# Optimization experiments

Hardware: AMD Instinct MI355X
Metric: run time of the kernel (lower is better)

Reference implementation:

```python
import jax, jax.numpy as jnp
import numpy as np

N = 50000
E = 625000
D_IN, D_HID, D_OUT = 128, 128, 64


def setup_inputs() -> dict:
    key = jax.random.key(0)
    k1, k2, k3, k4 = jax.random.split(key, 4)
    x = jax.random.normal(k1, (N, D_IN), dtype=jnp.float32)
    edge_index = jax.random.randint(k2, (2, E), 0, N, dtype=jnp.int32)
    # Glorot-ish init for linear weights (PyG lin has no bias; bias added after agg)
    W1 = jax.random.normal(k3, (D_HID, D_IN), dtype=jnp.float32) / np.sqrt(D_IN)
    b1 = jnp.zeros((D_HID,), dtype=jnp.float32)
    W2 = jax.random.normal(k4, (D_OUT, D_HID), dtype=jnp.float32) / np.sqrt(D_HID)
    b2 = jnp.zeros((D_OUT,), dtype=jnp.float32)
    return {"x": x, "edge_index": edge_index, "W1": W1, "b1": b1, "W2": W2, "b2": b2}


def _gcn_conv(x, W, b, src, dst, n):
    # GCNConv: h = x @ W^T; out[dst] += norm * h[src]; out += b
    # src/dst already include self-loops; symmetric normalization deg^{-1/2}.
    ones = jnp.ones(src.shape[0], dtype=x.dtype)
    deg = jax.ops.segment_sum(ones, dst, num_segments=n)
    dinv = jnp.where(deg > 0, jax.lax.rsqrt(deg), 0.0)
    norm = dinv[src] * dinv[dst]                      # [E+N]
    h = x @ W.T                                        # [N, d_out]
    msg = norm[:, None] * h[src]                       # [E+N, d_out]
    out = jax.ops.segment_sum(msg, dst, num_segments=n)
    return out + b


def reference(x, edge_index, W1, b1, W2, b2):
    n = x.shape[0]
    loops = jnp.arange(n, dtype=edge_index.dtype)
    src = jnp.concatenate([edge_index[0], loops])      # add self-loops
    dst = jnp.concatenate([edge_index[1], loops])
    h = _gcn_conv(x, W1, b1, src, dst, n)
    h = jax.nn.relu(h)
    out = _gcn_conv(h, W2, b2, src, dst, n)
    return out
```

## Files before the change

kernel.cpp:

```cpp
#include <hip/hip_runtime.h>
#include <hip/hip_bf16.h>


typedef __attribute__((ext_vector_type(8))) __bf16 bf16x8;
typedef __attribute__((ext_vector_type(8))) unsigned short ushort8;
typedef __attribute__((ext_vector_type(4))) float floatx4;

static __device__ __forceinline__ float bf2f(unsigned short s) {
    unsigned u = ((unsigned)s) << 16;
    return __builtin_bit_cast(float, u);
}
static __device__ __forceinline__ unsigned short f2bf(float f) {
    unsigned u = __builtin_bit_cast(unsigned, f);
    unsigned r = (u + 0x7FFFu + ((u >> 16) & 1u)) >> 16;
    return (unsigned short)r;
}
static __device__ __forceinline__ void ld8f(const void* p, size_t idx, int isbf, float* o) {
    if (isbf) {
        ushort8 t = __builtin_bit_cast(ushort8, *(const int4*)((const unsigned short*)p + idx));
        #pragma unroll
        for (int j = 0; j < 8; ++j) o[j] = bf2f(t[j]);
    } else {
        const float* f = (const float*)p + idx;
        float4 a = *(const float4*)f;
        float4 b = *(const float4*)(f + 4);
        o[0]=a.x; o[1]=a.y; o[2]=a.z; o[3]=a.w; o[4]=b.x; o[5]=b.y; o[6]=b.z; o[7]=b.w;
    }
}
static __device__ __forceinline__ int4 ld8frag(const void* p, size_t idx, int isbf) {
    if (isbf) {
        return *(const int4*)((const unsigned short*)p + idx);
    } else {
        const float* f = (const float*)p + idx;
        float4 a = *(const float4*)f;
        float4 b = *(const float4*)(f + 4);
        ushort8 t;
        t[0]=f2bf(a.x); t[1]=f2bf(a.y); t[2]=f2bf(a.z); t[3]=f2bf(a.w);
        t[4]=f2bf(b.x); t[5]=f2bf(b.y); t[6]=f2bf(b.z); t[7]=f2bf(b.w);
        return __builtin_bit_cast(int4, t);
    }
}
static __device__ __forceinline__ float bread(const void* p, int i, int isbf) {
    return isbf ? bf2f(((const unsigned short*)p)[i]) : ((const float*)p)[i];
}

__global__ void k_detect(const unsigned* __restrict__ xw, int* flag) {
    __shared__ int red[256];
    int t = threadIdx.x;
    int cnt = 0;
    #pragma unroll
    for (int i = 0; i < 16; ++i) {
        unsigned w = xw[t * 16 + i];
        unsigned exp = (w >> 7) & 0xFFu;
        cnt += (exp <= 0x84u) ? 1 : 0;
    }
    red[t] = cnt;
    __syncthreads();
    for (int s = 128; s > 0; s >>= 1) {
        if (t < s) red[t] += red[t + s];
        __syncthreads();
    }
    if (t == 0) flag[0] = (red[0] >= 3686) ? 1 : 0;
}

__global__ void k_zero(int* cnt, int n) {
    int i = blockIdx.x * 256 + threadIdx.x;
    if (i < n) cnt[i] = 0;
}
__global__ void k_count(const int* __restrict__ dst, int* __restrict__ cnt, int E) {
    int e = blockIdx.x * 256 + threadIdx.x;
    if (e < E) atomicAdd(&cnt[dst[e]], 1);
}
__global__ __launch_bounds__(1024) void k_scan(
    const int* __restrict__ cnt, int* __restrict__ off, int* __restrict__ cursor,
    float* __restrict__ dinv, int N)
{
    __shared__ int wtot[16];
    __shared__ int woff[16];
    __shared__ int s_carry;
    int t = threadIdx.x, lane = t & 63, wid = t >> 6;
    if (t == 0) s_carry = 0;
    __syncthreads();
    int nchunk = (N + 1023) / 1024;
    for (int c = 0; c < nchunk; ++c) {
        int i = c * 1024 + t;
        int v = (i < N) ? cnt[i] : 0;
        int x = v;
        #pragma unroll
        for (int s = 1; s < 64; s <<= 1) {
            int u = __shfl_up(x, s, 64);
            if (lane >= s) x += u;
        }
        if (lane == 63) wtot[wid] = x;
        __syncthreads();
        if (wid == 0) {
            int tv = (lane < 16) ? wtot[lane] : 0;
            int y = tv;
            #pragma unroll
            for (int s = 1; s < 16; s <<= 1) {
                int u = __shfl_up(y, s, 64);
                if (lane >= s) y += u;
            }
            if (lane < 16) woff[lane] = y - tv;
        }
        __syncthreads();
        int carry = s_carry;
        if (i < N) {
            int excl = carry + woff[wid] + (x - v);
            off[i] = excl;
            cursor[i] = excl;
            dinv[i] = rsqrtf(1.0f + (float)v);
        }
        __syncthreads();
        if (t == 0) s_carry = carry + woff[15] + wtot[15];
        __syncthreads();
    }
    if (t == 0) off[N] = s_carry;
}
__global__ void k_scatter(const int* __restrict__ src, const int* __restrict__ dst,
                          int* __restrict__ cursor, int* __restrict__ bucket, int E) {
    int e = blockIdx.x * 256 + threadIdx.x;
    if (e >= E) return;
    int pos = atomicAdd(&cursor[dst[e]], 1);
    bucket[pos] = src[e];
}

__global__ __launch_bounds__(256) void k_gather1(
    const void* __restrict__ x, const float* __restrict__ dinv,
    const int* __restrict__ off, const int* __restrict__ bucket,
    float* __restrict__ buf, int N, const int* __restrict__ flag)
{
    int isbf = *flag;
    int gid = blockIdx.x * 256 + threadIdx.x;
    int node = gid >> 4, p = gid & 15;
    if (node >= N) return;
    float di = dinv[node];
    float acc[8], v[8];
    ld8f(x, (size_t)node * 128 + p * 8, isbf, v);
    float w0 = di * di;
    #pragma unroll
    for (int j = 0; j < 8; ++j) acc[j] = w0 * v[j];
    int s0 = off[node], s1 = off[node + 1];
    for (int it = s0; it < s1; ++it) {
        int s = bucket[it];
        float w = di * dinv[s];
        ld8f(x, (size_t)s * 128 + p * 8, isbf, v);
        #pragma unroll
        for (int j = 0; j < 8; ++j) acc[j] += w * v[j];
    }
    float* o = &buf[(size_t)node * 128 + p * 8];
    float4 a = {acc[0], acc[1], acc[2], acc[3]};
    float4 b = {acc[4], acc[5], acc[6], acc[7]};
    *(float4*)o = a;
    *(float4*)(o + 4) = b;
}

__global__ __launch_bounds__(256) void k_gemm1(
    float* buf, const void* __restrict__ W1, const void* __restrict__ b1,
    int N, const int* __restrict__ flag)
{
    int isbf = *flag;
    __shared__ int4 lds[2048];
    int tid = threadIdx.x;
    for (int u = tid; u < 2048; u += 256) {
        int nt = u >> 8, kt = (u >> 6) & 3, lane = u & 63;
        int so = (nt * 16 + (lane & 15)) * 128 + kt * 32 + ((lane >> 4) << 3);
        lds[u] = ld8frag(W1, so, isbf);
    }
    __syncthreads();

    int wave = tid >> 6, lane = tid & 63;
    int ntile = (N + 15) >> 4;
    int tile = blockIdx.x * 4 + wave;
    if (tile >= ntile) return;
    int m = lane & 15, quad = lane >> 4;

    int arow = tile * 16 + m;
    if (arow >= N) arow = N - 1;
    bf16x8 a[4];
    for (int kt = 0; kt < 4; ++kt) {
        const float* p = &buf[(size_t)arow * 128 + kt * 32 + quad * 8];
        float4 f0 = *(const float4*)p;
        float4 f1 = *(const float4*)(p + 4);
        ushort8 t;
        t[0]=f2bf(f0.x); t[1]=f2bf(f0.y); t[2]=f2bf(f0.z); t[3]=f2bf(f0.w);
        t[4]=f2bf(f1.x); t[5]=f2bf(f1.y); t[6]=f2bf(f1.z); t[7]=f2bf(f1.w);
        a[kt] = __builtin_bit_cast(bf16x8, t);
    }

    floatx4 acc[8];
    floatx4 z = {0.f, 0.f, 0.f, 0.f};
    for (int nt = 0; nt < 8; ++nt) acc[nt] = z;
    for (int kt = 0; kt < 4; ++kt)
        for (int nt = 0; nt < 8; ++nt) {
            bf16x8 b = __builtin_bit_cast(bf16x8, lds[nt * 256 + kt * 64 + lane]);
            acc[nt] = __builtin_amdgcn_mfma_f32_16x16x32_bf16(a[kt], b, acc[nt], 0, 0, 0);
        }

    unsigned short* h1 = (unsigned short*)buf;
    int rbase = tile * 16 + quad * 4;
    for (int nt = 0; nt < 8; ++nt) {
        int col = nt * 16 + m;
        float bb = bread(b1, col, isbf);
        for (int r = 0; r < 4; ++r) {
            int orow = rbase + r;
            if (orow < N) {
                float v = acc[nt][r] + bb;
                h1[(size_t)orow * 256 + col] = f2bf(fmaxf(v, 0.f));
            }
        }
    }
}

__global__ __launch_bounds__(256) void k_gemm2(
    float* buf, const void* __restrict__ W2, int N, const int* __restrict__ flag)
{
    int isbf = *flag;
    __shared__ int4 lds[1024];
    int tid = threadIdx.x;
    for (int u = tid; u < 1024; u += 256) {
        int nt = u >> 8, kt = (u >> 6) & 3, lane = u & 63;
        int so = (nt * 16 + (lane & 15)) * 128 + kt * 32 + ((lane >> 4) << 3);
        lds[u] = ld8frag(W2, so, isbf);
    }
    __syncthreads();

    int wave = tid >> 6, lane = tid & 63;
    int ntile = (N + 15) >> 4;
    int tile = blockIdx.x * 4 + wave;
    if (tile >= ntile) return;
    int m = lane & 15, quad = lane >> 4;

    const unsigned short* h1 = (const unsigned short*)buf;
    int arow = tile * 16 + m;
    if (arow >= N) arow = N - 1;
    bf16x8 a[4];
    for (int kt = 0; kt < 4; ++kt)
        a[kt] = __builtin_bit_cast(bf16x8, *(const int4*)&h1[(size_t)arow * 256 + kt * 32 + quad * 8]);

    floatx4 acc[4];
    floatx4 z = {0.f, 0.f, 0.f, 0.f};
    for (int nt = 0; nt < 4; ++nt) acc[nt] = z;
    for (int kt = 0; kt < 4; ++kt)
        for (int nt = 0; nt < 4; ++nt) {
            bf16x8 b = __builtin_bit_cast(bf16x8, lds[nt * 256 + kt * 64 + lane]);
            acc[nt] = __builtin_amdgcn_mfma_f32_16x16x32_bf16(a[kt], b, acc[nt], 0, 0, 0);
        }

    unsigned short* h2 = (unsigned short*)buf;
    int rbase = tile * 16 + quad * 4;
    for (int nt = 0; nt < 4; ++nt) {
        int col = nt * 16 + m;
        for (int r = 0; r < 4; ++r) {
            int orow = rbase + r;
            if (orow < N)
                h2[(size_t)orow * 256 + col] = f2bf(acc[nt][r]);
        }
    }
}

__global__ __launch_bounds__(256) void k_gather2(
    const float* __restrict__ buf, const float* __restrict__ dinv,
    const int* __restrict__ off, const int* __restrict__ bucket,
    const void* __restrict__ b2, void* __restrict__ out, int N,
    const int* __restrict__ flag)
{
    int isbf = *flag;
    int gid = blockIdx.x * 256 + threadIdx.x;
    int node = gid >> 3, p = gid & 7;
    if (node >= N) return;
    const unsigned short* h2 = (const unsigned short*)buf;
    float di = dinv[node];
    float acc[8];
    {
        ushort8 t = __builtin_bit_cast(ushort8, *(const int4*)&h2[(size_t)node * 256 + p * 8]);
        float w0 = di * di;
        #pragma unroll
        for (int j = 0; j < 8; ++j) acc[j] = w0 * bf2f(t[j]);
    }
    int s0 = off[node], s1 = off[node + 1];
    for (int it = s0; it < s1; ++it) {
        int s = bucket[it];
        float w = di * dinv[s];
        ushort8 t = __builtin_bit_cast(ushort8, *(const int4*)&h2[(size_t)s * 256 + p * 8]);
        #pragma unroll
        for (int j = 0; j < 8; ++j) acc[j] += w * bf2f(t[j]);
    }
    #pragma unroll
    for (int j = 0; j < 8; ++j) acc[j] += bread(b2, p * 8 + j, isbf);
    if (isbf) {
        ushort8 o;
        #pragma unroll
        for (int j = 0; j < 8; ++j) o[j] = f2bf(acc[j]);
        *(int4*)((unsigned short*)out + (size_t)node * 64 + p * 8) = __builtin_bit_cast(int4, o);
    } else {
        float* fo = (float*)out + (size_t)node * 64 + p * 8;
        float4 a = {acc[0], acc[1], acc[2], acc[3]};
        float4 b = {acc[4], acc[5], acc[6], acc[7]};
        *(float4*)fo = a;
        *(float4*)(fo + 4) = b;
    }
}

extern "C" void kernel_launch(void* const* d_in, const int* in_sizes, int n_in,
                              void* d_out, int out_size, void* d_ws, size_t ws_size,
                              hipStream_t stream) {
    const void* x  = d_in[0];
    const int*  ei = (const int*)d_in[1];
    const void* W1 = d_in[2];
    const void* b1 = d_in[3];
    const void* W2 = d_in[4];
    const void* b2 = d_in[5];

    int N = in_sizes[0] / 128;
    int E = in_sizes[1] / 2;
    const int* srcI = ei;
    const int* dstI = ei + E;

    char* base = (char*)d_ws;
    size_t o = 0;
    auto take = [&](size_t bytes) { size_t r = o; o += (bytes + 255) & ~(size_t)255; return r; };
    int*   flag   = (int*)  (base + take(4));
    int*   cnt    = (int*)  (base + take((size_t)N * 4));
    int*   off    = (int*)  (base + take((size_t)(N + 1) * 4));
    int*   cursor = (int*)  (base + take((size_t)N * 4));
    float* dinv   = (float*)(base + take((size_t)N * 4));
    int*   bucket = (int*)  (base + take((size_t)E * 4));
    float* buf    = (float*)(base + take((size_t)N * 512));

    int ntile = (N + 15) / 16;
    int gemmBlocks = (ntile + 3) / 4;

    k_detect<<<1, 256, 0, stream>>>((const unsigned*)x, flag);
    k_zero<<<(N + 255) / 256, 256, 0, stream>>>(cnt, N);
    k_count<<<(E + 255) / 256, 256, 0, stream>>>(dstI, cnt, E);
    k_scan<<<1, 1024, 0, stream>>>(cnt, off, cursor, dinv, N);
    k_scatter<<<(E + 255) / 256, 256, 0, stream>>>(srcI, dstI, cursor, bucket, E);
    k_gather1<<<(N * 16 + 255) / 256, 256, 0, stream>>>(x, dinv, off, bucket, buf, N, flag);
    k_gemm1<<<gemmBlocks, 256, 0, stream>>>(buf, W1, b1, N, flag);
    k_gemm2<<<gemmBlocks, 256, 0, stream>>>(buf, W2, N, flag);
    k_gather2<<<(N * 8 + 255) / 256, 256, 0, stream>>>(buf, dinv, off, bucket, b2, d_out, N, flag);
}
```

Baseline: 298.1 us.

## Parallelize degree prefix scan across blocks and unroll gather loops by two

Replaces the single-block serial-chunk prefix scan over node degrees with a three-kernel reduce/scan/downsweep scheme spread across many blocks. Each thread now handles four elements. The neighbor gather loops in both aggregation kernels are unrolled by two so two independent row loads are in flight per iteration. This trades one long single-workgroup kernel for three short launches plus extra workspace, and raises register use in the gathers.

```diff
diff --git a/kernel.cpp b/kernel.cpp
--- a/kernel.cpp
+++ b/kernel.cpp
@@ -71,52 +71,88 @@
     int e = blockIdx.x * 256 + threadIdx.x;
     if (e < E) atomicAdd(&cnt[dst[e]], 1);
 }
-__global__ __launch_bounds__(1024) void k_scan(
-    const int* __restrict__ cnt, int* __restrict__ off, int* __restrict__ cursor,
-    float* __restrict__ dinv, int N)
-{
-    __shared__ int wtot[16];
-    __shared__ int woff[16];
-    __shared__ int s_carry;
-    int t = threadIdx.x, lane = t & 63, wid = t >> 6;
-    if (t == 0) s_carry = 0;
-    __syncthreads();
-    int nchunk = (N + 1023) / 1024;
-    for (int c = 0; c < nchunk; ++c) {
-        int i = c * 1024 + t;
-        int v = (i < N) ? cnt[i] : 0;
+
+__global__ __launch_bounds__(256) void k_scanA(
+    const int* __restrict__ cnt, int* __restrict__ partial, int N)
+{
+    int b = blockIdx.x, t = threadIdx.x;
+    int base = b * 1024 + t * 4;
+    int s = 0;
+    if (base + 3 < N) {
+        int4 v = *(const int4*)&cnt[base];
+        s = v.x + v.y + v.z + v.w;
+    } else {
+        for (int j = 0; j < 4; ++j) { int i = base + j; if (i < N) s += cnt[i]; }
+    }
+    #pragma unroll
+    for (int d = 1; d < 64; d <<= 1) s += __shfl_down(s, d, 64);
+    __shared__ int ws[4];
+    int lane = t & 63, wid = t >> 6;
+    if (lane == 0) ws[wid] = s;
+    __syncthreads();
+    if (t == 0) partial[b] = ws[0] + ws[1] + ws[2] + ws[3];
+}
+__global__ void k_scanB(const int* __restrict__ partial, int* __restrict__ prefix, int nb) {
+    int lane = threadIdx.x;
+    int carry = 0;
+    int nch = (nb + 63) / 64;
+    for (int c = 0; c < nch; ++c) {
+        int i = c * 64 + lane;
+        int v = (i < nb) ? partial[i] : 0;
         int x = v;
         #pragma unroll
-        for (int s = 1; s < 64; s <<= 1) {
-            int u = __shfl_up(x, s, 64);
-            if (lane >= s) x += u;
-        }
-        if (lane == 63) wtot[wid] = x;
-        __syncthreads();
-        if (wid == 0) {
-            int tv = (lane < 16) ? wtot[lane] : 0;
-            int y = tv;
-            #pragma unroll
-            for (int s = 1; s < 16; s <<= 1) {
-                int u = __shfl_up(y, s, 64);
-                if (lane >= s) y += u;
-            }
-            if (lane < 16) woff[lane] = y - tv;
-        }
-        __syncthreads();
-        int carry = s_carry;
+        for (int d = 1; d < 64; d <<= 1) {
+            int u = __shfl_up(x, d, 64);
+            if (lane >= d) x += u;
+        }
+        if (i < nb) prefix[i] = carry + x - v;
+        carry += __shfl(x, 63, 64);
+    }
+    if (lane == 0) prefix[nb] = carry;
+}
+__global__ __launch_bounds__(256) void k_scanC(
+    const int* __restrict__ cnt, const int* __restrict__ prefix,
+    int* __restrict__ off, int* __restrict__ cursor, float* __restrict__ dinv,
+    int N, int nb)
+{
+    int b = blockIdx.x, t = threadIdx.x, lane = t & 63, wid = t >> 6;
+    int base = b * 1024 + t * 4;
+    int v[4], s = 0;
+    #pragma unroll
+    for (int j = 0; j < 4; ++j) {
+        int i = base + j;
+        v[j] = (i < N) ? cnt[i] : 0;
+        s += v[j];
+    }
+    int x = s;
+    #pragma unroll
+    for (int d = 1; d < 64; d <<= 1) {
+        int u = __shfl_up(x, d, 64);
+        if (lane >= d) x += u;
+    }
+    __shared__ int wtot[4], woff[4];
+    if (lane == 63) wtot[wid] = x;
+    __syncthreads();
+    if (t == 0) {
+        int a = 0;
+        #pragma unroll
+        for (int w = 0; w < 4; ++w) { woff[w] = a; a += wtot[w]; }
+    }
+    __syncthreads();
+    int excl = prefix[b] + woff[wid] + (x - s);
+    #pragma unroll
+    for (int j = 0; j < 4; ++j) {
+        int i = base + j;
         if (i < N) {
-            int excl = carry + woff[wid] + (x - v);
             off[i] = excl;
             cursor[i] = excl;
-            dinv[i] = rsqrtf(1.0f + (float)v);
-        }
-        __syncthreads();
-        if (t == 0) s_carry = carry + woff[15] + wtot[15];
-        __syncthreads();
-    }
-    if (t == 0) off[N] = s_carry;
-}
+            dinv[i] = rsqrtf(1.0f + (float)v[j]);
+            excl += v[j];
+        }
+    }
+    if (b == 0 && t == 0) off[N] = prefix[nb];
+}
+
 __global__ void k_scatter(const int* __restrict__ src, const int* __restrict__ dst,
                           int* __restrict__ cursor, int* __restrict__ bucket, int E) {
     int e = blockIdx.x * 256 + threadIdx.x;
@@ -135,18 +171,26 @@
     int node = gid >> 4, p = gid & 15;
     if (node >= N) return;
     float di = dinv[node];
-    float acc[8], v[8];
-    ld8f(x, (size_t)node * 128 + p * 8, isbf, v);
+    float acc[8], va[8], vb[8];
+    ld8f(x, (size_t)node * 128 + p * 8, isbf, va);
     float w0 = di * di;
     #pragma unroll
-    for (int j = 0; j < 8; ++j) acc[j] = w0 * v[j];
-    int s0 = off[node], s1 = off[node + 1];
-    for (int it = s0; it < s1; ++it) {
-        int s = bucket[it];
-        float w = di * dinv[s];
-        ld8f(x, (size_t)s * 128 + p * 8, isbf, v);
-        #pragma unroll
-        for (int j = 0; j < 8; ++j) acc[j] += w * v[j];
+    for (int j = 0; j < 8; ++j) acc[j] = w0 * va[j];
+    int it = off[node], s1 = off[node + 1];
+    for (; it + 1 < s1; it += 2) {
+        int sa = bucket[it], sb = bucket[it + 1];
+        float wa = di * dinv[sa], wb = di * dinv[sb];
+        ld8f(x, (size_t)sa * 128 + p * 8, isbf, va);
+        ld8f(x, (size_t)sb * 128 + p * 8, isbf, vb);
+        #pragma unroll
+        for (int j = 0; j < 8; ++j) acc[j] += wa * va[j] + wb * vb[j];
+    }
+    if (it < s1) {
+        int sa = bucket[it];
+        float wa = di * dinv[sa];
+        ld8f(x, (size_t)sa * 128 + p * 8, isbf, va);
+        #pragma unroll
+        for (int j = 0; j < 8; ++j) acc[j] += wa * va[j];
     }
     float* o = &buf[(size_t)node * 128 + p * 8];
     float4 a = {acc[0], acc[1], acc[2], acc[3]};
@@ -278,13 +322,21 @@
         #pragma unroll
         for (int j = 0; j < 8; ++j) acc[j] = w0 * bf2f(t[j]);
     }
-    int s0 = off[node], s1 = off[node + 1];
-    for (int it = s0; it < s1; ++it) {
-        int s = bucket[it];
-        float w = di * dinv[s];
-        ushort8 t = __builtin_bit_cast(ushort8, *(const int4*)&h2[(size_t)s * 256 + p * 8]);
-        #pragma unroll
-        for (int j = 0; j < 8; ++j) acc[j] += w * bf2f(t[j]);
+    int it = off[node], s1 = off[node + 1];
+    for (; it + 1 < s1; it += 2) {
+        int sa = bucket[it], sb = bucket[it + 1];
+        float wa = di * dinv[sa], wb = di * dinv[sb];
+        ushort8 ta = __builtin_bit_cast(ushort8, *(const int4*)&h2[(size_t)sa * 256 + p * 8]);
+        ushort8 tb = __builtin_bit_cast(ushort8, *(const int4*)&h2[(size_t)sb * 256 + p * 8]);
+        #pragma unroll
+        for (int j = 0; j < 8; ++j) acc[j] += wa * bf2f(ta[j]) + wb * bf2f(tb[j]);
+    }
+    if (it < s1) {
+        int sa = bucket[it];
+        float wa = di * dinv[sa];
+        ushort8 ta = __builtin_bit_cast(ushort8, *(const int4*)&h2[(size_t)sa * 256 + p * 8]);
+        #pragma unroll
+        for (int j = 0; j < 8; ++j) acc[j] += wa * bf2f(ta[j]);
     }
     #pragma unroll
     for (int j = 0; j < 8; ++j) acc[j] += bread(b2, p * 8 + j, isbf);
@@ -317,16 +369,20 @@
     const int* srcI = ei;
     const int* dstI = ei + E;
 
+    int nb = (N + 1023) / 1024;
+
     char* base = (char*)d_ws;
     size_t o = 0;
     auto take = [&](size_t bytes) { size_t r = o; o += (bytes + 255) & ~(size_t)255; return r; };
-    int*   flag   = (int*)  (base + take(4));
-    int*   cnt    = (int*)  (base + take((size_t)N * 4));
-    int*   off    = (int*)  (base + take((size_t)(N + 1) * 4));
-    int*   cursor = (int*)  (base + take((size_t)N * 4));
-    float* dinv   = (float*)(base + take((size_t)N * 4));
-    int*   bucket = (int*)  (base + take((size_t)E * 4));
-    float* buf    = (float*)(base + take((size_t)N * 512));
+    int*   flag    = (int*)  (base + take(4));
+    int*   cnt     = (int*)  (base + take((size_t)N * 4));
+    int*   off     = (int*)  (base + take((size_t)(N + 1) * 4));
+    int*   cursor  = (int*)  (base + take((size_t)N * 4));
+    float* dinv    = (float*)(base + take((size_t)N * 4));
+    int*   partial = (int*)  (base + take((size_t)nb * 4));
+    int*   prefix  = (int*)  (base + take((size_t)(nb + 1) * 4));
+    int*   bucket  = (int*)  (base + take((size_t)E * 4));
+    float* buf     = (float*)(base + take((size_t)N * 512));
 
     int ntile = (N + 15) / 16;
     int gemmBlocks = (ntile + 3) / 4;
@@ -334,7 +390,9 @@
     k_detect<<<1, 256, 0, stream>>>((const unsigned*)x, flag);
     k_zero<<<(N + 255) / 256, 256, 0, stream>>>(cnt, N);
     k_count<<<(E + 255) / 256, 256, 0, stream>>>(dstI, cnt, E);
-    k_scan<<<1, 1024, 0, stream>>>(cnt, off, cursor, dinv, N);
+    k_scanA<<<nb, 256, 0, stream>>>(cnt, partial, N);
+    k_scanB<<<1, 64, 0, stream>>>(partial, prefix, nb);
+    k_scanC<<<nb, 256, 0, stream>>>(cnt, prefix, off, cursor, dinv, N, nb);
     k_scatter<<<(E + 255) / 256, 256, 0, stream>>>(srcI, dstI, cursor, bucket, E);
     k_gather1<<<(N * 16 + 255) / 256, 256, 0, stream>>>(x, dinv, off, bucket, buf, N, flag);
     k_gemm1<<<gemmBlocks, 256, 0, stream>>>(buf, W1, b1, N, flag);
```

After: 246.6 us. 1.21x faster.
